# Kernel tuning notes

Hardware: AMD Instinct MI355X
Metric: run time of the kernel (lower is better)

## Reference

```python
import jax, jax.numpy as jnp
import numpy as np

D_MODEL = 1024
N_HEADS = 16
DEPTH = D_MODEL // N_HEADS
NEG_INF = -1.0e9


def setup_inputs() -> dict:
    key = jax.random.key(0)
    ks = jax.random.split(key, 11)
    B, S = 2, 2048
    xk = jax.random.normal(ks[0], (B, S, D_MODEL), jnp.float32)
    xq = jax.random.normal(ks[1], (B, S, D_MODEL), jnp.float32)
    xv = jax.random.normal(ks[2], (B, S, D_MODEL), jnp.float32)
    sc = 1.0 / np.sqrt(D_MODEL)
    wq = jax.random.normal(ks[3], (D_MODEL, D_MODEL), jnp.float32) * sc
    wk = jax.random.normal(ks[4], (D_MODEL, D_MODEL), jnp.float32) * sc
    wv = jax.random.normal(ks[5], (D_MODEL, D_MODEL), jnp.float32) * sc
    wo = jax.random.normal(ks[6], (D_MODEL, D_MODEL), jnp.float32) * sc
    bq = jnp.zeros((D_MODEL,), jnp.float32)
    bk = jnp.zeros((D_MODEL,), jnp.float32)
    bv = jnp.zeros((D_MODEL,), jnp.float32)
    bo = jnp.zeros((D_MODEL,), jnp.float32)
    return {"xk": xk, "xq": xq, "xv": xv, "wq": wq, "bq": bq, "wk": wk,
            "bk": bk, "wv": wv, "bv": bv, "wo": wo, "bo": bo}


def _split_heads(t):
    # [B, S, D] -> [B, H, S, depth]
    B, S, _ = t.shape
    return t.reshape(B, S, N_HEADS, DEPTH).transpose(0, 2, 1, 3)


def reference(xk, xq, xv, wq, bq, wk, bk, wv, bv, wo, bo):
    B, Sq, _ = xq.shape
    Sk = xk.shape[1]
    q = _split_heads(xq @ wq + bq)  # [B,H,Sq,d]
    k = _split_heads(xk @ wk + bk)  # [B,H,Sk,d]
    v = _split_heads(xv @ wv + bv)  # [B,H,Sk,d]
    logits = jnp.einsum('bhqd,bhkd->bhqk', q, k) / jnp.sqrt(
        jnp.asarray(DEPTH, q.dtype))
    # additive causal mask: (1 - lower_triangular) * -1e9
    causal = (1.0 - jnp.tril(jnp.ones((Sq, Sk), logits.dtype))) * NEG_INF
    logits = logits + causal[None, None, :, :]
    attn = jax.nn.softmax(logits, axis=-1)
    out = jnp.einsum('bhqk,bhkd->bhqd', attn, v)
    out = out.transpose(0, 2, 1, 3).reshape(B, Sq, D_MODEL)
    return out @ wo + bo
```

## Files before the change

kernel.cpp:

```cpp
#include <hip/hip_runtime.h>

typedef unsigned short u16;
typedef u16 u16x8 __attribute__((ext_vector_type(8)));
typedef __bf16 bf16x8 __attribute__((ext_vector_type(8)));
typedef float f32x4 __attribute__((ext_vector_type(4)));

#define DM 1024
#define SEQ 2048
#define BATCH 2
#define MROWS 4096

__device__ __forceinline__ u16 f2bf(float f) {
  unsigned int x = __builtin_bit_cast(unsigned int, f);
  x += 0x7fffu + ((x >> 16) & 1u);
  return (u16)(x >> 16);
}
__device__ __forceinline__ u16 f2bf_trunc(float f) {
  return (u16)(__builtin_bit_cast(unsigned int, f) >> 16);
}

__device__ __forceinline__ void gld16(const void* g, void* l) {
  __builtin_amdgcn_global_load_lds(
      (const __attribute__((address_space(1))) void*)g,
      (__attribute__((address_space(3))) void*)l, 16, 0, 0);
}

struct TrArgs { const float* in[4]; u16* out[4]; };

__global__ __launch_bounds__(256) void transpose_w4(TrArgs a) {
  const float* __restrict__ in = a.in[blockIdx.z];
  u16* __restrict__ out = a.out[blockIdx.z];
  __shared__ u16 T[64][72];
  int r0 = blockIdx.y * 64, c0 = blockIdx.x * 64;
  int t = threadIdx.x;
  int r = t >> 3, cg = (t & 7) * 8;
#pragma unroll
  for (int p = 0; p < 2; p++) {
    const float* src = in + (size_t)(r0 + r + p * 32) * DM + c0 + cg;
    f32x4 x0 = *(const f32x4*)src;
    f32x4 x1 = *(const f32x4*)(src + 4);
    u16x8 v;
#pragma unroll
    for (int j = 0; j < 4; j++) { v[j] = f2bf(x0[j]); v[4 + j] = f2bf(x1[j]); }
    *(u16x8*)(&T[r + p * 32][cg]) = v;
  }
  __syncthreads();
#pragma unroll
  for (int p = 0; p < 2; p++) {
    int orow = r + p * 32;
    u16x8 v;
#pragma unroll
    for (int j = 0; j < 8; j++) v[j] = T[cg + j][orow];
    *(u16x8*)(out + (size_t)(c0 + orow) * DM + r0 + cg) = v;
  }
}

struct CastArgs { const float* in[3]; u16* out[3]; };

__global__ __launch_bounds__(256) void cast_x(CastArgs a) {
  const float* __restrict__ in = a.in[blockIdx.y];
  u16* __restrict__ out = a.out[blockIdx.y];
  size_t e = ((size_t)blockIdx.x * 256 + threadIdx.x) * 8;
  f32x4 a0 = *(const f32x4*)(in + e);
  f32x4 a1 = *(const f32x4*)(in + e + 4);
  u16x8 v;
#pragma unroll
  for (int j = 0; j < 4; j++) { v[j] = f2bf(a0[j]); v[4 + j] = f2bf(a1[j]); }
  *(u16x8*)(out + e) = v;
}

struct GemmArgs { const void* A[3]; const u16* WT[3]; const float* bias[3]; void* C[3]; };

template <int MT, int NT, bool AF32, bool OF32>
__global__ __launch_bounds__(256) void gemmT(GemmArgs g) {
  __shared__ __align__(16) u16 As[MT * 32 * 32];
  __shared__ __align__(16) u16 Bs[NT * 32 * 32];
  const int z = blockIdx.z;
  const u16* __restrict__ WT = g.WT[z];
  const int tid = threadIdx.x;
  const int lane = tid & 63, wave = tid >> 6;
  const int fr = lane & 15, kq = lane >> 4;
  const int mq = (wave >> 1) * (MT * 16), nq = (wave & 1) * (NT * 16);
  const int m0 = blockIdx.y * (MT * 32), n0 = blockIdx.x * (NT * 32);
  const int srow = tid >> 2;
  const int scA = ((tid & 3) ^ ((srow >> 1) & 3)) * 8;
  const int fco = ((kq ^ ((fr >> 1) & 3)) * 8);
  f32x4 acc[MT][NT] = {};

  for (int kk = 0; kk < DM; kk += 32) {
    __syncthreads();
    if constexpr (AF32) {
      const float* A = (const float*)g.A[z];
#pragma unroll
      for (int i = 0; i < MT / 2; i++) {
        const float* s0 = A + (size_t)(m0 + i * 64 + srow) * DM + kk + scA;
        f32x4 a0 = *(const f32x4*)s0, a1 = *(const f32x4*)(s0 + 4);
        u16x8 v;
#pragma unroll
        for (int j = 0; j < 4; j++) { v[j] = f2bf(a0[j]); v[4 + j] = f2bf(a1[j]); }
        *(u16x8*)(As + (i * 256 + tid) * 8) = v;
      }
    } else {
      const u16* A = (const u16*)g.A[z];
#pragma unroll
      for (int i = 0; i < MT / 2; i++)
        gld16(A + (size_t)(m0 + i * 64 + srow) * DM + kk + scA,
              As + (i * 256 + tid) * 8);
    }
#pragma unroll
    for (int i = 0; i < NT / 2; i++)
      gld16(WT + (size_t)(n0 + i * 64 + srow) * DM + kk + scA,
            Bs + (i * 256 + tid) * 8);
    __syncthreads();
    bf16x8 af[MT], bfr[NT];
#pragma unroll
    for (int mt = 0; mt < MT; mt++)
      af[mt] = __builtin_bit_cast(
          bf16x8, *(const u16x8*)(As + (mq + mt * 16 + fr) * 32 + fco));
#pragma unroll
    for (int nt = 0; nt < NT; nt++)
      bfr[nt] = __builtin_bit_cast(
          bf16x8, *(const u16x8*)(Bs + (nq + nt * 16 + fr) * 32 + fco));
#pragma unroll
    for (int mt = 0; mt < MT; mt++)
#pragma unroll
      for (int nt = 0; nt < NT; nt++)
        acc[mt][nt] =
            __builtin_amdgcn_mfma_f32_16x16x32_bf16(af[mt], bfr[nt], acc[mt][nt], 0, 0, 0);
  }
  const float* __restrict__ bias = g.bias[z];
#pragma unroll
  for (int nt = 0; nt < NT; nt++) {
    int col = n0 + nq + nt * 16 + fr;
    float bb = bias[col];
#pragma unroll
    for (int mt = 0; mt < MT; mt++)
#pragma unroll
      for (int r = 0; r < 4; r++) {
        int row = m0 + mq + mt * 16 + kq * 4 + r;
        float val = acc[mt][nt][r] + bb;
        if constexpr (OF32)
          ((float*)g.C[z])[(size_t)row * DM + col] = val;
        else
          ((u16*)g.C[z])[(size_t)row * DM + col] = f2bf(val);
      }
  }
}

#define KS 72
__global__ __launch_bounds__(256) void attn3(u16* __restrict__ Q,
                                             const u16* __restrict__ K,
                                             const u16* __restrict__ V) {
  __shared__ __align__(16) u16 Ksh[64 * 64];
  __shared__ __align__(16) u16 Vt[80 * KS];
  __shared__ __align__(16) u16 Ps[4][16 * KS];
  const int tid = threadIdx.x, wave = tid >> 6, lane = tid & 63;
  const int fr = lane & 15, kq = lane >> 4;
  const int b = blockIdx.x >> 4, h = blockIdx.x & 15;
  const int qt = 31 - blockIdx.y;
  const float C1 = 0.125f * 1.44269504f;

#pragma unroll
  for (int i = 0; i < 4; i++) {
    int e = tid * 4 + i;
    int rr = e >> 6, cc = e & 63;
    Vt[(64 + rr) * KS + cc] = (rr == 0) ? (u16)0x3F80 : (u16)0;
  }

  const int krow = tid >> 3;
  const int kcs = ((tid & 7) ^ (krow & 7)) * 8;
  const int f7 = fr & 7;
  const int x0 = (kq ^ f7) * 8;
  const int x1 = ((4 + kq) ^ f7) * 8;

  bf16x8 qf0, qf1;
  {
    size_t qr = (size_t)(b * SEQ + qt * 64 + wave * 16 + fr) * DM + h * 64;
    qf0 = __builtin_bit_cast(bf16x8, *(const u16x8*)(Q + qr + kq * 8));
    qf1 = __builtin_bit_cast(bf16x8, *(const u16x8*)(Q + qr + 32 + kq * 8));
  }

  f32x4 ov[5] = {};
  u16* Pw = Ps[wave];

  for (int t = 0; t <= qt; t++) {
    __syncthreads();
    {
      size_t gk = (size_t)(b * SEQ + t * 64 + krow) * DM + h * 64 + kcs;
      gld16(K + gk, Ksh + tid * 8);
      gld16(K + gk + (size_t)32 * DM, Ksh + (256 + tid) * 8);
      size_t gv = (size_t)(b * SEQ + t * 64 + lane) * DM + h * 64 + wave * 16;
      u16x8 v0 = *(const u16x8*)(V + gv);
      u16x8 v1 = *(const u16x8*)(V + gv + 8);
#pragma unroll
      for (int j = 0; j < 8; j++) {
        Vt[(wave * 16 + j) * KS + lane] = v0[j];
        Vt[(wave * 16 + 8 + j) * KS + lane] = v1[j];
      }
    }
    __syncthreads();
    f32x4 sv[4];
#pragma unroll
    for (int nt = 0; nt < 4; nt++) {
      f32x4 s = {};
      bf16x8 b0 = __builtin_bit_cast(
          bf16x8, *(const u16x8*)(Ksh + (nt * 16 + fr) * 64 + x0));
      s = __builtin_amdgcn_mfma_f32_16x16x32_bf16(qf0, b0, s, 0, 0, 0);
      bf16x8 b1 = __builtin_bit_cast(
          bf16x8, *(const u16x8*)(Ksh + (nt * 16 + fr) * 64 + x1));
      s = __builtin_amdgcn_mfma_f32_16x16x32_bf16(qf1, b1, s, 0, 0, 0);
      sv[nt] = s;
    }
    if (t == qt) {
#pragma unroll
      for (int nt = 0; nt < 4; nt++)
#pragma unroll
        for (int r = 0; r < 4; r++)
          if (nt * 16 + fr > wave * 16 + kq * 4 + r) sv[nt][r] = -1e30f;
    }
#pragma unroll
    for (int nt = 0; nt < 4; nt++)
#pragma unroll
      for (int r = 0; r < 4; r++) {
        float pp = __builtin_amdgcn_exp2f(sv[nt][r] * C1);
        Pw[(kq * 4 + r) * KS + nt * 16 + fr] = f2bf_trunc(pp);
      }
#pragma unroll
    for (int kk = 0; kk < 2; kk++) {
      bf16x8 pa = __builtin_bit_cast(
          bf16x8, *(const u16x8*)(Pw + fr * KS + kk * 32 + kq * 8));
#pragma unroll
      for (int nt = 0; nt < 5; nt++) {
        bf16x8 vb = __builtin_bit_cast(
            bf16x8, *(const u16x8*)(Vt + (nt * 16 + fr) * KS + kk * 32 + kq * 8));
        ov[nt] = __builtin_amdgcn_mfma_f32_16x16x32_bf16(pa, vb, ov[nt], 0, 0, 0);
      }
    }
  }
  float rinv[4];
#pragma unroll
  for (int r = 0; r < 4; r++) rinv[r] = 1.0f / __shfl(ov[4][r], lane & 48);
#pragma unroll
  for (int nt = 0; nt < 4; nt++)
#pragma unroll
    for (int r = 0; r < 4; r++) {
      int row = qt * 64 + wave * 16 + kq * 4 + r;
      Q[(size_t)(b * SEQ + row) * DM + h * 64 + nt * 16 + fr] =
          f2bf(ov[nt][r] * rinv[r]);
    }
}

extern "C" void kernel_launch(void* const* d_in, const int* in_sizes, int n_in,
                              void* d_out, int out_size, void* d_ws,
                              size_t ws_size, hipStream_t stream) {
  const float* xk = (const float*)d_in[0];
  const float* xq = (const float*)d_in[1];
  const float* xv = (const float*)d_in[2];
  const float* wq = (const float*)d_in[3];
  const float* bq = (const float*)d_in[4];
  const float* wk = (const float*)d_in[5];
  const float* bk = (const float*)d_in[6];
  const float* wv = (const float*)d_in[7];
  const float* bv = (const float*)d_in[8];
  const float* wo = (const float*)d_in[9];
  const float* bo = (const float*)d_in[10];

  u16* Qb = (u16*)d_ws;
  u16* Kb = Qb + (size_t)MROWS * DM;
  u16* Vb = Kb + (size_t)MROWS * DM;
  u16* WTq = Vb + (size_t)MROWS * DM;
  u16* WTk = WTq + (size_t)DM * DM;
  u16* WTv = WTk + (size_t)DM * DM;
  u16* WTo = WTv + (size_t)DM * DM;
  u16* Xq = WTo + (size_t)DM * DM;
  u16* Xk = Xq + (size_t)MROWS * DM;
  u16* Xv = Xk + (size_t)MROWS * DM;
  const bool cast_path =
      ws_size >= ((size_t)(3 * 8 + 4 * 2 + 3 * 8)) * 1024 * 1024;

  dim3 blk(256);

  TrArgs tr;
  tr.in[0] = wq; tr.in[1] = wk; tr.in[2] = wv; tr.in[3] = wo;
  tr.out[0] = WTq; tr.out[1] = WTk; tr.out[2] = WTv; tr.out[3] = WTo;
  transpose_w4<<<dim3(16, 16, 4), blk, 0, stream>>>(tr);

  GemmArgs gq;
  gq.WT[0] = WTq; gq.WT[1] = WTk; gq.WT[2] = WTv;
  gq.bias[0] = bq; gq.bias[1] = bk; gq.bias[2] = bv;
  gq.C[0] = Qb; gq.C[1] = Kb; gq.C[2] = Vb;
  if (cast_path) {
    CastArgs ca;
    ca.in[0] = xq; ca.in[1] = xk; ca.in[2] = xv;
    ca.out[0] = Xq; ca.out[1] = Xk; ca.out[2] = Xv;
    cast_x<<<dim3(MROWS * DM / 2048, 3), blk, 0, stream>>>(ca);
    gq.A[0] = Xq; gq.A[1] = Xk; gq.A[2] = Xv;
    gemmT<4, 4, false, false>
        <<<dim3(DM / 128, MROWS / 128, 3), blk, 0, stream>>>(gq);
  } else {
    gq.A[0] = xq; gq.A[1] = xk; gq.A[2] = xv;
    gemmT<4, 4, true, false>
        <<<dim3(DM / 128, MROWS / 128, 3), blk, 0, stream>>>(gq);
  }

  attn3<<<dim3(BATCH * 16, 32), blk, 0, stream>>>(Qb, Kb, Vb);

  GemmArgs go;
  go.A[0] = Qb;  go.WT[0] = WTo; go.bias[0] = bo; go.C[0] = d_out;
  go.A[1] = Qb;  go.WT[1] = WTo; go.bias[1] = bo; go.C[1] = d_out;
  go.A[2] = Qb;  go.WT[2] = WTo; go.bias[2] = bo; go.C[2] = d_out;
  gemmT<2, 4, false, true>
      <<<dim3(DM / 128, MROWS / 64, 1), blk, 0, stream>>>(go);
}
```

Baseline: 225.4 us.

## Double-buffer K/V tiles in attention and use all-ones register operand for row sums

Double-buffers the K and V shared-memory tiles. The next tile's K loads (async to LDS) and V global loads are issued before the current tile's compute, and the V transpose store is deferred until after the PV MFMAs. This cuts one barrier per iteration and hides global load latency behind the MFMAs. The row-sum column is now computed with an all-ones register B operand rather than padded LDS rows, which removes the shuffle in the normalisation. The cost is more LDS and registers held across the loop, which may lower occupancy.

```diff
diff --git a/kernel.cpp b/kernel.cpp
--- a/kernel.cpp
+++ b/kernel.cpp
@@ -151,8 +151,8 @@
 __global__ __launch_bounds__(256) void attn3(u16* __restrict__ Q,
                                              const u16* __restrict__ K,
                                              const u16* __restrict__ V) {
-  __shared__ __align__(16) u16 Ksh[64 * 64];
-  __shared__ __align__(16) u16 Vt[80 * KS];
+  __shared__ __align__(16) u16 Ksh[2][64 * 64];
+  __shared__ __align__(16) u16 Vt[2][64 * KS];
   __shared__ __align__(16) u16 Ps[4][16 * KS];
   const int tid = threadIdx.x, wave = tid >> 6, lane = tid & 63;
   const int fr = lane & 15, kq = lane >> 4;
@@ -160,15 +160,11 @@
   const int qt = 31 - blockIdx.y;
   const float C1 = 0.125f * 1.44269504f;
 
-#pragma unroll
-  for (int i = 0; i < 4; i++) {
-    int e = tid * 4 + i;
-    int rr = e >> 6, cc = e & 63;
-    Vt[(64 + rr) * KS + cc] = (rr == 0) ? (u16)0x3F80 : (u16)0;
-  }
-
   const int krow = tid >> 3;
   const int kcs = ((tid & 7) ^ (krow & 7)) * 8;
+  const u16* Kg = K + (size_t)(b * SEQ + krow) * DM + h * 64 + kcs;
+  const u16* Vg = V + (size_t)(b * SEQ + lane) * DM + h * 64 + wave * 16;
+
   const int f7 = fr & 7;
   const int x0 = (kq ^ f7) * 8;
   const int x1 = ((4 + kq) ^ f7) * 8;
@@ -180,34 +176,49 @@
     qf1 = __builtin_bit_cast(bf16x8, *(const u16x8*)(Q + qr + 32 + kq * 8));
   }
 
+  u16x8 onesu;
+#pragma unroll
+  for (int j = 0; j < 8; j++) onesu[j] = 0x3F80;
+  const bf16x8 vones = __builtin_bit_cast(bf16x8, onesu);
+
   f32x4 ov[5] = {};
   u16* Pw = Ps[wave];
 
+  gld16(Kg, Ksh[0] + tid * 8);
+  gld16(Kg + (size_t)32 * DM, Ksh[0] + (256 + tid) * 8);
+  {
+    u16x8 v0 = *(const u16x8*)(Vg);
+    u16x8 v1 = *(const u16x8*)(Vg + 8);
+#pragma unroll
+    for (int j = 0; j < 8; j++) {
+      Vt[0][(wave * 16 + j) * KS + lane] = v0[j];
+      Vt[0][(wave * 16 + 8 + j) * KS + lane] = v1[j];
+    }
+  }
+  __syncthreads();
+
+  int cur = 0;
   for (int t = 0; t <= qt; t++) {
-    __syncthreads();
-    {
-      size_t gk = (size_t)(b * SEQ + t * 64 + krow) * DM + h * 64 + kcs;
-      gld16(K + gk, Ksh + tid * 8);
-      gld16(K + gk + (size_t)32 * DM, Ksh + (256 + tid) * 8);
-      size_t gv = (size_t)(b * SEQ + t * 64 + lane) * DM + h * 64 + wave * 16;
-      u16x8 v0 = *(const u16x8*)(V + gv);
-      u16x8 v1 = *(const u16x8*)(V + gv + 8);
-#pragma unroll
-      for (int j = 0; j < 8; j++) {
-        Vt[(wave * 16 + j) * KS + lane] = v0[j];
-        Vt[(wave * 16 + 8 + j) * KS + lane] = v1[j];
-      }
-    }
-    __syncthreads();
+    const int nb = cur ^ 1;
+    u16x8 nv0, nv1;
+    const bool pf = (t < qt);
+    if (pf) {
+      size_t ro = (size_t)(t + 1) * 64 * DM;
+      gld16(Kg + ro, Ksh[nb] + tid * 8);
+      gld16(Kg + ro + (size_t)32 * DM, Ksh[nb] + (256 + tid) * 8);
+      nv0 = *(const u16x8*)(Vg + ro);
+      nv1 = *(const u16x8*)(Vg + ro + 8);
+    }
+    const u16* Kc = Ksh[cur];
     f32x4 sv[4];
 #pragma unroll
     for (int nt = 0; nt < 4; nt++) {
       f32x4 s = {};
       bf16x8 b0 = __builtin_bit_cast(
-          bf16x8, *(const u16x8*)(Ksh + (nt * 16 + fr) * 64 + x0));
+          bf16x8, *(const u16x8*)(Kc + (nt * 16 + fr) * 64 + x0));
       s = __builtin_amdgcn_mfma_f32_16x16x32_bf16(qf0, b0, s, 0, 0, 0);
       bf16x8 b1 = __builtin_bit_cast(
-          bf16x8, *(const u16x8*)(Ksh + (nt * 16 + fr) * 64 + x1));
+          bf16x8, *(const u16x8*)(Kc + (nt * 16 + fr) * 64 + x1));
       s = __builtin_amdgcn_mfma_f32_16x16x32_bf16(qf1, b1, s, 0, 0, 0);
       sv[nt] = s;
     }
@@ -225,21 +236,32 @@
         float pp = __builtin_amdgcn_exp2f(sv[nt][r] * C1);
         Pw[(kq * 4 + r) * KS + nt * 16 + fr] = f2bf_trunc(pp);
       }
+    const u16* Vc = Vt[cur];
 #pragma unroll
     for (int kk = 0; kk < 2; kk++) {
       bf16x8 pa = __builtin_bit_cast(
           bf16x8, *(const u16x8*)(Pw + fr * KS + kk * 32 + kq * 8));
 #pragma unroll
-      for (int nt = 0; nt < 5; nt++) {
+      for (int nt = 0; nt < 4; nt++) {
         bf16x8 vb = __builtin_bit_cast(
-            bf16x8, *(const u16x8*)(Vt + (nt * 16 + fr) * KS + kk * 32 + kq * 8));
+            bf16x8, *(const u16x8*)(Vc + (nt * 16 + fr) * KS + kk * 32 + kq * 8));
         ov[nt] = __builtin_amdgcn_mfma_f32_16x16x32_bf16(pa, vb, ov[nt], 0, 0, 0);
       }
-    }
+      ov[4] = __builtin_amdgcn_mfma_f32_16x16x32_bf16(pa, vones, ov[4], 0, 0, 0);
+    }
+    if (pf) {
+#pragma unroll
+      for (int j = 0; j < 8; j++) {
+        Vt[nb][(wave * 16 + j) * KS + lane] = nv0[j];
+        Vt[nb][(wave * 16 + 8 + j) * KS + lane] = nv1[j];
+      }
+    }
+    __syncthreads();
+    cur = nb;
   }
   float rinv[4];
 #pragma unroll
-  for (int r = 0; r < 4; r++) rinv[r] = 1.0f / __shfl(ov[4][r], lane & 48);
+  for (int r = 0; r < 4; r++) rinv[r] = 1.0f / ov[4][r];
 #pragma unroll
   for (int nt = 0; nt < 4; nt++)
 #pragma unroll
```

After: 219.2 us. -2.7%, faster.
